# Kernel tuning notes

Measured on AMD Instinct MI355X. Metric: run time of the kernel, lower is better.

The kernel has to match this reference:

```python
import jax, jax.numpy as jnp
import numpy as np

B, T, D_IN = 4096, 1024, 2
EMD, CELL, D_OUT = 128, 128, 5


def setup_inputs() -> dict:
    key = jax.random.key(0)
    ks = jax.random.split(key, 9)
    s = lambda k, shape, fan: jax.random.normal(k, shape, jnp.float32) / np.sqrt(fan)
    return {
        "inputs": jax.random.normal(ks[0], (B, T, D_IN), jnp.float32),
        "We": s(ks[1], (EMD, D_IN), D_IN),
        "be": s(ks[2], (EMD,), D_IN),
        "W_ih": s(ks[3], (4 * CELL, EMD), EMD),
        "W_hh": s(ks[4], (4 * CELL, CELL), CELL),
        "b_ih": s(ks[5], (4 * CELL,), CELL),
        "b_hh": s(ks[6], (4 * CELL,), CELL),
        "Wo": s(ks[7], (D_OUT, CELL), CELL),
        "bo": s(ks[8], (D_OUT,), CELL),
    }


def reference(inputs, We, be, W_ih, W_hh, b_ih, b_hh, Wo, bo):
    """VanillaLSTM forward: per-step embed MLP -> LSTMCell -> output MLP.
    inputs: [B, T, D_IN]; returns (outputs [B, T, D_OUT], h [B,CELL], c [B,CELL])."""
    Bsz = inputs.shape[0]
    cell = W_hh.shape[1]

    def step(hc, x_t):
        h, c = hc
        # input embedding MLP (Linear + ReLU, batch_norm=False)
        e = jax.nn.relu(x_t @ We.T + be)                      # [B, EMD]
        # torch.nn.LSTMCell gate math
        gates = e @ W_ih.T + b_ih + h @ W_hh.T + b_hh         # [B, 4*CELL]
        i, f, g, o = jnp.split(gates, 4, axis=-1)
        i, f, o = jax.nn.sigmoid(i), jax.nn.sigmoid(f), jax.nn.sigmoid(o)
        g = jnp.tanh(g)
        c_new = f * c + i * g
        h_new = o * jnp.tanh(c_new)
        # output embedding (Linear, no activation)
        y = h_new @ Wo.T + bo                                 # [B, D_OUT]
        return (h_new, c_new), y

    h0 = jnp.zeros((Bsz, cell), inputs.dtype)
    c0 = jnp.zeros((Bsz, cell), inputs.dtype)
    xs = jnp.swapaxes(inputs, 0, 1)                           # [T, B, D_IN]
    (h, c), ys = jax.lax.scan(step, (h0, c0), xs)
    outputs = jnp.swapaxes(ys, 0, 1)                          # [B, T, D_OUT]
    return outputs, h, c
```

## Files before the change

kernel.cpp:

```cpp
#include <hip/hip_runtime.h>
#include <hip/hip_bf16.h>
#include <type_traits>


#define B_TOT 4096
#define T_LEN 1024
#define D_INP 2
#define EMD   128
#define CELL  128
#define D_OUT 5

#define ROWS  16
#define WAVES 8
#define BLOCK (WAVES * 64)
#define LDH   136

typedef short s8v  __attribute__((ext_vector_type(8)));
typedef float f32x4 __attribute__((ext_vector_type(4)));

#define BAR() asm volatile("s_waitcnt lgkmcnt(0)\n\ts_barrier" ::: "memory")

#if __has_builtin(__builtin_amdgcn_exp2f)
#define EXP2F(x) __builtin_amdgcn_exp2f(x)
#else
#define EXP2F(x) exp2f(x)
#endif
#if __has_builtin(__builtin_amdgcn_rcpf)
#define RCPF(x) __builtin_amdgcn_rcpf(x)
#else
#define RCPF(x) (1.0f / (x))
#endif

__device__ __forceinline__ short f2bf(float f) {
    unsigned int u = __builtin_bit_cast(unsigned int, f);
    u += 0x7fffu + ((u >> 16) & 1u);
    return (short)(u >> 16);
}
__device__ __forceinline__ unsigned int pk2(float a, float b) {
    unsigned int ua = __builtin_bit_cast(unsigned int, a) + 0x8000u;
    unsigned int ub = __builtin_bit_cast(unsigned int, b) + 0x8000u;
    return __builtin_amdgcn_perm(ub, ua, 0x07060302);
}
__device__ __forceinline__ s8v load8_scaled(const float* p, float s) {
    float4 a = *(const float4*)p;
    float4 b = *(const float4*)(p + 4);
    s8v r;
    r[0] = f2bf(a.x * s); r[1] = f2bf(a.y * s); r[2] = f2bf(a.z * s); r[3] = f2bf(a.w * s);
    r[4] = f2bf(b.x * s); r[5] = f2bf(b.y * s); r[6] = f2bf(b.z * s); r[7] = f2bf(b.w * s);
    return r;
}

__global__ __launch_bounds__(BLOCK, 1)
void lstm_persistent(const float* __restrict__ x,
                     const float* __restrict__ We,
                     const float* __restrict__ be,
                     const float* __restrict__ Wih,
                     const float* __restrict__ Whh,
                     const float* __restrict__ bih,
                     const float* __restrict__ bhh,
                     const float* __restrict__ Wo,
                     const float* __restrict__ bo,
                     float* __restrict__ out)
{
    __shared__ short h_lds[2][ROWS][LDH];
    __shared__ short e_lds[2][ROWS][LDH];

    const int tid  = threadIdx.x;
    const int lane = tid & 63;
    const int w    = tid >> 6;
    const int n16  = lane & 15;
    const int q    = lane >> 4;
    const int q8   = q * 8;
    const int b0   = blockIdx.x * ROWS;
    const int ch0  = w * 16 + q * 4;

    float* out_y = out;
    float* out_h = out + (size_t)B_TOT * T_LEN * D_OUT;
    float* out_c = out_h + (size_t)B_TOT * CELL;

    const float GSC[4] = {-1.44269504f, -1.44269504f, -2.88539008f, -1.44269504f};

    s8v wih_f[4][4], whh_f[4][4];
    #pragma unroll
    for (int g = 0; g < 4; ++g) {
        const int row = g * CELL + w * 16 + n16;
        #pragma unroll
        for (int kt = 0; kt < 4; ++kt) {
            wih_f[g][kt] = load8_scaled(Wih + row * EMD  + kt * 32 + q8, GSC[g]);
            whh_f[g][kt] = load8_scaled(Whh + row * CELL + kt * 32 + q8, GSC[g]);
        }
    }
    float4 bias4[4];
    #pragma unroll
    for (int g = 0; g < 4; ++g) {
        float4 bi = *(const float4*)(bih + g * CELL + ch0);
        float4 bh = *(const float4*)(bhh + g * CELL + ch0);
        bias4[g] = make_float4((bi.x + bh.x) * GSC[g], (bi.y + bh.y) * GSC[g],
                               (bi.z + bh.z) * GSC[g], (bi.w + bh.w) * GSC[g]);
    }

    s8v wo_f[4];
    float bo_r[4];
    {
        s8v z = {0, 0, 0, 0, 0, 0, 0, 0};
        #pragma unroll
        for (int kt = 0; kt < 4; ++kt) wo_f[kt] = z;
        if (w == 0 && n16 < D_OUT) {
            #pragma unroll
            for (int kt = 0; kt < 4; ++kt)
                wo_f[kt] = load8_scaled(Wo + n16 * CELL + kt * 32 + q8, 1.0f);
        }
        #pragma unroll
        for (int r = 0; r < 4; ++r) {
            const int oc = q * 4 + r;
            bo_r[r] = (w == 0 && oc < D_OUT) ? bo[oc] : 0.0f;
        }
    }

    const int er  = tid >> 5;
    const int jj0 = (tid & 31) * 4;
    float weA[4], weB[4], bev[4];
    #pragma unroll
    for (int jl = 0; jl < 4; ++jl) {
        weA[jl] = We[(jj0 + jl) * 2 + 0];
        weB[jl] = We[(jj0 + jl) * 2 + 1];
        bev[jl] = be[jj0 + jl];
    }
    const float* xrow = x + (size_t)(b0 + er) * T_LEN * D_INP;

    {
        unsigned int* hz = (unsigned int*)&h_lds[0][0][0];
        for (int i = tid; i < ROWS * LDH / 2; i += BLOCK) hz[i] = 0u;

        float2 xd = *(const float2*)(xrow);
        float e0 = fmaxf(xd.x * weA[0] + xd.y * weB[0] + bev[0], 0.0f);
        float e1 = fmaxf(xd.x * weA[1] + xd.y * weB[1] + bev[1], 0.0f);
        float e2 = fmaxf(xd.x * weA[2] + xd.y * weB[2] + bev[2], 0.0f);
        float e3 = fmaxf(xd.x * weA[3] + xd.y * weB[3] + bev[3], 0.0f);
        unsigned int* ep = (unsigned int*)&e_lds[0][er][jj0];
        ep[0] = pk2(e0, e1); ep[1] = pk2(e2, e3);
    }

    float c_r[4] = {0.0f, 0.0f, 0.0f, 0.0f};

    auto step = [&](int u, auto Pc) {
        constexpr int P = decltype(Pc)::value;
        BAR();

        const int tn = (u + 1) & (T_LEN - 1);
        float2 xd = *(const float2*)(xrow + tn * D_INP);

        s8v ah[4], ae[4];
        #pragma unroll
        for (int kt = 0; kt < 4; ++kt) {
            ah[kt] = *(const s8v*)&h_lds[P][n16][kt * 32 + q8];
            ae[kt] = *(const s8v*)&e_lds[P][n16][kt * 32 + q8];
        }

        const bool ydo = (w == 0) && (u > 0);
        f32x4 ay;
        if (ydo) {
            ay = f32x4{bo_r[0], bo_r[1], bo_r[2], bo_r[3]};
            #pragma unroll
            for (int kt = 0; kt < 4; ++kt)
                ay = __builtin_amdgcn_mfma_f32_16x16x32_bf16(wo_f[kt], ah[kt], ay, 0, 0, 0);
        }

        f32x4 acc[4];
        #pragma unroll
        for (int g = 0; g < 4; ++g) {
            f32x4 a = {bias4[g].x, bias4[g].y, bias4[g].z, bias4[g].w};
            #pragma unroll
            for (int kt = 0; kt < 4; ++kt)
                a = __builtin_amdgcn_mfma_f32_16x16x32_bf16(wih_f[g][kt], ae[kt], a, 0, 0, 0);
            #pragma unroll
            for (int kt = 0; kt < 4; ++kt)
                a = __builtin_amdgcn_mfma_f32_16x16x32_bf16(whh_f[g][kt], ah[kt], a, 0, 0, 0);
            acc[g] = a;
        }

        float hv[4];
        #pragma unroll
        for (int r = 0; r < 4; ++r) {
            float ti = EXP2F(acc[0][r]);
            float tf = EXP2F(acc[1][r]);
            float tg = EXP2F(acc[2][r]);
            float to = EXP2F(acc[3][r]);
            float pig = (1.0f + ti) * (1.0f + tg);
            float pf  = 1.0f + tf;
            float num = c_r[r] * pig + pf * (1.0f - tg);
            float rd  = RCPF(pf * pig);
            float cn  = num * rd;
            c_r[r] = cn;
            float tc = EXP2F(-2.88539008f * cn);
            float rh = RCPF((1.0f + to) * (1.0f + tc));
            hv[r] = (1.0f - tc) * rh;
        }
        {
            unsigned int* hp = (unsigned int*)&h_lds[1 - P][n16][ch0];
            hp[0] = pk2(hv[0], hv[1]); hp[1] = pk2(hv[2], hv[3]);
        }
        if (u == T_LEN - 1) {
            *(float4*)(out_h + (size_t)(b0 + n16) * CELL + ch0) =
                make_float4(hv[0], hv[1], hv[2], hv[3]);
        }
        {
            float e0 = fmaxf(xd.x * weA[0] + xd.y * weB[0] + bev[0], 0.0f);
            float e1 = fmaxf(xd.x * weA[1] + xd.y * weB[1] + bev[1], 0.0f);
            float e2 = fmaxf(xd.x * weA[2] + xd.y * weB[2] + bev[2], 0.0f);
            float e3 = fmaxf(xd.x * weA[3] + xd.y * weB[3] + bev[3], 0.0f);
            unsigned int* ep = (unsigned int*)&e_lds[1 - P][er][jj0];
            ep[0] = pk2(e0, e1); ep[1] = pk2(e2, e3);
        }

        if (ydo) {
            float* yp = out_y + ((size_t)(b0 + n16) * T_LEN + (u - 1)) * D_OUT;
            if (q == 0) { yp[0] = ay[0]; yp[1] = ay[1]; yp[2] = ay[2]; yp[3] = ay[3]; }
            else if (q == 1) { yp[4] = ay[0]; }
        }
    };

    #pragma unroll 1
    for (int u = 0; u < T_LEN; u += 2) {
        step(u,     std::integral_constant<int, 0>{});
        step(u + 1, std::integral_constant<int, 1>{});
    }

    BAR();

    if (w == 0) {
        s8v ah[4];
        #pragma unroll
        for (int kt = 0; kt < 4; ++kt)
            ah[kt] = *(const s8v*)&h_lds[0][n16][kt * 32 + q8];
        f32x4 ay = {bo_r[0], bo_r[1], bo_r[2], bo_r[3]};
        #pragma unroll
        for (int kt = 0; kt < 4; ++kt)
            ay = __builtin_amdgcn_mfma_f32_16x16x32_bf16(wo_f[kt], ah[kt], ay, 0, 0, 0);
        float* yp = out_y + ((size_t)(b0 + n16) * T_LEN + (T_LEN - 1)) * D_OUT;
        if (q == 0) {
            yp[0] = ay[0]; yp[1] = ay[1]; yp[2] = ay[2]; yp[3] = ay[3];
        } else if (q == 1) {
            yp[4] = ay[0];
        }
    }

    *(float4*)(out_c + (size_t)(b0 + n16) * CELL + ch0) =
        make_float4(c_r[0], c_r[1], c_r[2], c_r[3]);
}

extern "C" void kernel_launch(void* const* d_in, const int* in_sizes, int n_in,
                              void* d_out, int out_size, void* d_ws, size_t ws_size,
                              hipStream_t stream) {
    const float* x   = (const float*)d_in[0];
    const float* We  = (const float*)d_in[1];
    const float* be  = (const float*)d_in[2];
    const float* Wih = (const float*)d_in[3];
    const float* Whh = (const float*)d_in[4];
    const float* bih = (const float*)d_in[5];
    const float* bhh = (const float*)d_in[6];
    const float* Wo  = (const float*)d_in[7];
    const float* bo  = (const float*)d_in[8];
    float* out = (float*)d_out;

    dim3 grid(B_TOT / ROWS);
    dim3 block(BLOCK);
    hipLaunchKernelGGL(lstm_persistent, grid, block, 0, stream,
                       x, We, be, Wih, Whh, bih, bhh, Wo, bo, out);
}
```

Baseline: 1.248 ms.

## Precompute next step's input-gate MFMAs and interleave them with gate activations

Moves the W_ih·e contribution for step t+1 off the recurrent critical path. It is computed during step t and interleaved with the transcendental gate math, so each step only issues the 16 W_hh MFMAs after the barrier. The embedding is now produced two steps ahead, and the e buffer indexing is shifted to match. This adds four live accumulator vectors and a prologue step, which raises register pressure.

```diff
diff --git a/kernel.cpp b/kernel.cpp
--- a/kernel.cpp
+++ b/kernel.cpp
@@ -19,6 +19,7 @@
 typedef float f32x4 __attribute__((ext_vector_type(4)));
 
 #define BAR() asm volatile("s_waitcnt lgkmcnt(0)\n\ts_barrier" ::: "memory")
+#define MFMA_BF16(A, B, C) __builtin_amdgcn_mfma_f32_16x16x32_bf16((A), (B), (C), 0, 0, 0)
 
 #if __has_builtin(__builtin_amdgcn_exp2f)
 #define EXP2F(x) __builtin_amdgcn_exp2f(x)
@@ -90,17 +91,17 @@
             whh_f[g][kt] = load8_scaled(Whh + row * CELL + kt * 32 + q8, GSC[g]);
         }
     }
-    float4 bias4[4];
+    f32x4 bias_v[4];
     #pragma unroll
     for (int g = 0; g < 4; ++g) {
         float4 bi = *(const float4*)(bih + g * CELL + ch0);
         float4 bh = *(const float4*)(bhh + g * CELL + ch0);
-        bias4[g] = make_float4((bi.x + bh.x) * GSC[g], (bi.y + bh.y) * GSC[g],
-                               (bi.z + bh.z) * GSC[g], (bi.w + bh.w) * GSC[g]);
+        bias_v[g] = f32x4{(bi.x + bh.x) * GSC[g], (bi.y + bh.y) * GSC[g],
+                          (bi.z + bh.z) * GSC[g], (bi.w + bh.w) * GSC[g]};
     }
 
     s8v wo_f[4];
-    float bo_r[4];
+    f32x4 bo_v;
     {
         s8v z = {0, 0, 0, 0, 0, 0, 0, 0};
         #pragma unroll
@@ -113,7 +114,7 @@
         #pragma unroll
         for (int r = 0; r < 4; ++r) {
             const int oc = q * 4 + r;
-            bo_r[r] = (w == 0 && oc < D_OUT) ? bo[oc] : 0.0f;
+            bo_v[r] = (w == 0 && oc < D_OUT) ? bo[oc] : 0.0f;
         }
     }
 
@@ -128,17 +129,38 @@
     }
     const float* xrow = x + (size_t)(b0 + er) * T_LEN * D_INP;
 
-    {
-        unsigned int* hz = (unsigned int*)&h_lds[0][0][0];
-        for (int i = tid; i < ROWS * LDH / 2; i += BLOCK) hz[i] = 0u;
-
-        float2 xd = *(const float2*)(xrow);
+    auto embed = [&](int t, short (*ebuf)[LDH]) {
+        float2 xd = *(const float2*)(xrow + t * D_INP);
         float e0 = fmaxf(xd.x * weA[0] + xd.y * weB[0] + bev[0], 0.0f);
         float e1 = fmaxf(xd.x * weA[1] + xd.y * weB[1] + bev[1], 0.0f);
         float e2 = fmaxf(xd.x * weA[2] + xd.y * weB[2] + bev[2], 0.0f);
         float e3 = fmaxf(xd.x * weA[3] + xd.y * weB[3] + bev[3], 0.0f);
-        unsigned int* ep = (unsigned int*)&e_lds[0][er][jj0];
+        unsigned int* ep = (unsigned int*)&ebuf[er][jj0];
         ep[0] = pk2(e0, e1); ep[1] = pk2(e2, e3);
+    };
+
+    {
+        unsigned int* hz = (unsigned int*)&h_lds[0][0][0];
+        for (int i = tid; i < ROWS * LDH / 2; i += BLOCK) hz[i] = 0u;
+        embed(0, e_lds[1]);
+    }
+    BAR();
+
+    f32x4 acc_e[4];
+    {
+        s8v ae0[4];
+        #pragma unroll
+        for (int kt = 0; kt < 4; ++kt)
+            ae0[kt] = *(const s8v*)&e_lds[1][n16][kt * 32 + q8];
+        #pragma unroll
+        for (int g = 0; g < 4; ++g) {
+            f32x4 a = MFMA_BF16(wih_f[g][0], ae0[0], bias_v[g]);
+            a = MFMA_BF16(wih_f[g][1], ae0[1], a);
+            a = MFMA_BF16(wih_f[g][2], ae0[2], a);
+            a = MFMA_BF16(wih_f[g][3], ae0[3], a);
+            acc_e[g] = a;
+        }
+        embed(1, e_lds[0]);
     }
 
     float c_r[4] = {0.0f, 0.0f, 0.0f, 0.0f};
@@ -147,9 +169,6 @@
         constexpr int P = decltype(Pc)::value;
         BAR();
 
-        const int tn = (u + 1) & (T_LEN - 1);
-        float2 xd = *(const float2*)(xrow + tn * D_INP);
-
         s8v ah[4], ae[4];
         #pragma unroll
         for (int kt = 0; kt < 4; ++kt) {
@@ -160,42 +179,45 @@
         const bool ydo = (w == 0) && (u > 0);
         f32x4 ay;
         if (ydo) {
-            ay = f32x4{bo_r[0], bo_r[1], bo_r[2], bo_r[3]};
-            #pragma unroll
-            for (int kt = 0; kt < 4; ++kt)
-                ay = __builtin_amdgcn_mfma_f32_16x16x32_bf16(wo_f[kt], ah[kt], ay, 0, 0, 0);
+            ay = MFMA_BF16(wo_f[0], ah[0], bo_v);
+            ay = MFMA_BF16(wo_f[1], ah[1], ay);
+            ay = MFMA_BF16(wo_f[2], ah[2], ay);
+            ay = MFMA_BF16(wo_f[3], ah[3], ay);
         }
 
         f32x4 acc[4];
         #pragma unroll
         for (int g = 0; g < 4; ++g) {
-            f32x4 a = {bias4[g].x, bias4[g].y, bias4[g].z, bias4[g].w};
-            #pragma unroll
-            for (int kt = 0; kt < 4; ++kt)
-                a = __builtin_amdgcn_mfma_f32_16x16x32_bf16(wih_f[g][kt], ae[kt], a, 0, 0, 0);
-            #pragma unroll
-            for (int kt = 0; kt < 4; ++kt)
-                a = __builtin_amdgcn_mfma_f32_16x16x32_bf16(whh_f[g][kt], ah[kt], a, 0, 0, 0);
+            f32x4 a = MFMA_BF16(whh_f[g][0], ah[0], acc_e[g]);
+            a = MFMA_BF16(whh_f[g][1], ah[1], a);
+            a = MFMA_BF16(whh_f[g][2], ah[2], a);
+            a = MFMA_BF16(whh_f[g][3], ah[3], a);
             acc[g] = a;
         }
 
         float hv[4];
         #pragma unroll
         for (int r = 0; r < 4; ++r) {
+            f32x4 a = MFMA_BF16(wih_f[r][0], ae[0], bias_v[r]);
             float ti = EXP2F(acc[0][r]);
             float tf = EXP2F(acc[1][r]);
             float tg = EXP2F(acc[2][r]);
             float to = EXP2F(acc[3][r]);
+            a = MFMA_BF16(wih_f[r][1], ae[1], a);
             float pig = (1.0f + ti) * (1.0f + tg);
             float pf  = 1.0f + tf;
             float num = c_r[r] * pig + pf * (1.0f - tg);
             float rd  = RCPF(pf * pig);
+            a = MFMA_BF16(wih_f[r][2], ae[2], a);
             float cn  = num * rd;
             c_r[r] = cn;
             float tc = EXP2F(-2.88539008f * cn);
+            a = MFMA_BF16(wih_f[r][3], ae[3], a);
             float rh = RCPF((1.0f + to) * (1.0f + tc));
             hv[r] = (1.0f - tc) * rh;
-        }
+            acc_e[r] = a;
+        }
+
         {
             unsigned int* hp = (unsigned int*)&h_lds[1 - P][n16][ch0];
             hp[0] = pk2(hv[0], hv[1]); hp[1] = pk2(hv[2], hv[3]);
@@ -204,14 +226,7 @@
             *(float4*)(out_h + (size_t)(b0 + n16) * CELL + ch0) =
                 make_float4(hv[0], hv[1], hv[2], hv[3]);
         }
-        {
-            float e0 = fmaxf(xd.x * weA[0] + xd.y * weB[0] + bev[0], 0.0f);
-            float e1 = fmaxf(xd.x * weA[1] + xd.y * weB[1] + bev[1], 0.0f);
-            float e2 = fmaxf(xd.x * weA[2] + xd.y * weB[2] + bev[2], 0.0f);
-            float e3 = fmaxf(xd.x * weA[3] + xd.y * weB[3] + bev[3], 0.0f);
-            unsigned int* ep = (unsigned int*)&e_lds[1 - P][er][jj0];
-            ep[0] = pk2(e0, e1); ep[1] = pk2(e2, e3);
-        }
+        embed((u + 2) & (T_LEN - 1), e_lds[1 - P]);
 
         if (ydo) {
             float* yp = out_y + ((size_t)(b0 + n16) * T_LEN + (u - 1)) * D_OUT;
@@ -233,10 +248,10 @@
         #pragma unroll
         for (int kt = 0; kt < 4; ++kt)
             ah[kt] = *(const s8v*)&h_lds[0][n16][kt * 32 + q8];
-        f32x4 ay = {bo_r[0], bo_r[1], bo_r[2], bo_r[3]};
-        #pragma unroll
-        for (int kt = 0; kt < 4; ++kt)
-            ay = __builtin_amdgcn_mfma_f32_16x16x32_bf16(wo_f[kt], ah[kt], ay, 0, 0, 0);
+        f32x4 ay = MFMA_BF16(wo_f[0], ah[0], bo_v);
+        ay = MFMA_BF16(wo_f[1], ah[1], ay);
+        ay = MFMA_BF16(wo_f[2], ah[2], ay);
+        ay = MFMA_BF16(wo_f[3], ah[3], ay);
         float* yp = out_y + ((size_t)(b0 + n16) * T_LEN + (T_LEN - 1)) * D_OUT;
         if (q == 0) {
             yp[0] = ay[0]; yp[1] = ay[1]; yp[2] = ay[2]; yp[3] = ay[3];
```

New measurement: 1.223 ms. -2.0%, faster.
